# Performance work log

Measured on AMD Instinct MI355X. Metric: run time of the kernel, lower is better.

## Reference

```python
import jax, jax.numpy as jnp
import numpy as np

B, S, D = 8, 2048, 1024
H = 16
DH = D // H  # 64
DFF = 4 * D
EPS = 1e-5


def setup_inputs() -> dict:
    key = jax.random.key(0)
    ks = jax.random.split(key, 12)
    s = 0.02
    x = jax.random.normal(ks[0], (B, S, D), dtype=jnp.float32)
    mask = jnp.ones((B, S), dtype=bool)
    Wq = jax.random.normal(ks[1], (H, D, DH), dtype=jnp.float32) * s
    Wk = jax.random.normal(ks[2], (H, D, DH), dtype=jnp.float32) * s
    Wv = jax.random.normal(ks[3], (H, D, DH), dtype=jnp.float32) * s
    bq = jnp.zeros((H, DH), dtype=jnp.float32)
    bk = jnp.zeros((H, DH), dtype=jnp.float32)
    bv = jnp.zeros((H, DH), dtype=jnp.float32)
    Wo = jax.random.normal(ks[4], (D, D), dtype=jnp.float32) * s
    bo = jnp.zeros((D,), dtype=jnp.float32)
    W1 = jax.random.normal(ks[5], (D, DFF), dtype=jnp.float32) * s
    b1 = jnp.zeros((DFF,), dtype=jnp.float32)
    W2 = jax.random.normal(ks[6], (DFF, D), dtype=jnp.float32) * s
    b2 = jnp.zeros((D,), dtype=jnp.float32)
    ln1_w = jnp.ones((D,), dtype=jnp.float32)
    ln1_b = jnp.zeros((D,), dtype=jnp.float32)
    ln2_w = jnp.ones((D,), dtype=jnp.float32)
    ln2_b = jnp.zeros((D,), dtype=jnp.float32)
    return dict(x=x, mask=mask, Wq=Wq, bq=bq, Wk=Wk, bk=bk, Wv=Wv, bv=bv,
                Wo=Wo, bo=bo, W1=W1, b1=b1, W2=W2, b2=b2,
                ln1_w=ln1_w, ln1_b=ln1_b, ln2_w=ln2_w, ln2_b=ln2_b)


def _layernorm(x, w, b):
    m = jnp.mean(x, axis=-1, keepdims=True)
    v = jnp.mean(jnp.square(x - m), axis=-1, keepdims=True)
    return (x - m) * jax.lax.rsqrt(v + EPS) * w + b


def _mha(h, mask, Wq, bq, Wk, bk, Wv, bv, Wo, bo):
    # batched per-head projections: [B,S,D] x [H,D,DH] -> [B,H,S,DH]
    q = jnp.einsum('bsd,hde->bhse', h, Wq) + bq[None, :, None, :]
    k = jnp.einsum('bsd,hde->bhse', h, Wk) + bk[None, :, None, :]
    v = jnp.einsum('bsd,hde->bhse', h, Wv) + bv[None, :, None, :]
    scores = jnp.einsum('bhse,bhte->bhst', q, k) / np.sqrt(DH).astype(np.float32)
    scores = jnp.where(mask[:, None, None, :], scores, -1e9)
    w = jax.nn.softmax(scores, axis=-1)
    o = jnp.einsum('bhst,bhte->bhse', w, v)           # [B,H,S,DH]
    o = o.transpose(0, 2, 1, 3).reshape(o.shape[0], o.shape[2], -1)  # concat heads -> [B,S,D]
    return o @ Wo + bo


def reference(x, mask, Wq, bq, Wk, bk, Wv, bv, Wo, bo, W1, b1, W2, b2,
              ln1_w, ln1_b, ln2_w, ln2_b):
    h = _layernorm(x, ln1_w, ln1_b)
    x = x + _mha(h, mask, Wq, bq, Wk, bk, Wv, bv, Wo, bo)
    h2 = _layernorm(x, ln2_w, ln2_b)
    ff = jax.nn.gelu(h2 @ W1 + b1, approximate=False) @ W2 + b2  # dropout is identity in eval
    return x + ff
```

## Files before the change

### kernel.cpp

```cpp
#include <hip/hip_runtime.h>
#include <hip/hip_bf16.h>

#define DEV __device__ __forceinline__

typedef __attribute__((ext_vector_type(8))) short short8;
typedef __attribute__((ext_vector_type(4))) float floatx4;
typedef __attribute__((ext_vector_type(4))) short short4_t;
typedef __attribute__((ext_vector_type(4))) int int4_t;
typedef __attribute__((ext_vector_type(4))) float f4_t;

constexpr int S_ = 2048;
constexpr int D_ = 1024;
constexpr int M_ = 8 * 2048;
constexpr long QKV_ONE = 16384L * 1024L;

constexpr float QSCALE = 0.18033688011112042f;
constexpr float EXP2_BIAS = 5.770780163555851f;

DEV short f2bf(float f) {
  __hip_bfloat16 h = __float2bfloat16(f);
  return __builtin_bit_cast(short, h);
}

DEV int cvt_pk_bf16(float lo, float hi) {
  int r;
  asm("v_cvt_pk_bf16_f32 %0, %1, %2" : "=v"(r) : "v"(lo), "v"(hi));
  return r;
}

DEV void async16(const void* g, void* l) {
  __builtin_amdgcn_global_load_lds((const __attribute__((address_space(1))) void*)g,
                                   (__attribute__((address_space(3))) void*)l, 16, 0, 0);
}

DEV float gelu_exact(float x) {
  return 0.5f * x * (1.f + erff(x * 0.70710678118654752f));
}

#define SB0 __builtin_amdgcn_sched_barrier(0)
#define BARX { SB0; __builtin_amdgcn_s_barrier(); SB0; }
#define LGKM0 { asm volatile("s_waitcnt lgkmcnt(0)" ::: "memory"); SB0; }
#define WAITV(N) { asm volatile("s_waitcnt vmcnt(" #N ")" ::: "memory"); SB0; }


__global__ void pack_qkv_w(const float* __restrict__ Wq, const float* __restrict__ Wk,
                           const float* __restrict__ Wv, short* __restrict__ dst) {
  int idx = blockIdx.x * 256 + threadIdx.x;
  if (idx >= 3072 * 1024) return;
  int n = idx >> 10, k = idx & 1023;
  int which = n >> 10, hh = (n >> 6) & 15, e = n & 63;
  const float* W = (which == 0) ? Wq : ((which == 1) ? Wk : Wv);
  dst[idx] = f2bf(W[(hh * 1024 + k) * 64 + e]);
}

__global__ void pack_transpose(const float* __restrict__ src, short* __restrict__ dst,
                               int R, int C) {
  int idx = blockIdx.x * 256 + threadIdx.x;
  if (idx >= R * C) return;
  int r = idx % R, c = idx / R;
  dst[idx] = f2bf(src[(size_t)r * C + c]);
}

__global__ void pack_bias(const float* __restrict__ bq, const float* __restrict__ bk,
                          const float* __restrict__ bv, float* __restrict__ dst) {
  int idx = blockIdx.x * 256 + threadIdx.x;
  if (idx >= 3072) return;
  int which = idx >> 10;
  const float* b = (which == 0) ? bq : ((which == 1) ? bk : bv);
  dst[idx] = b[idx & 1023];
}


__global__ __launch_bounds__(256) void ln_kernel(const float* __restrict__ x,
                                                 const float* __restrict__ w,
                                                 const float* __restrict__ b,
                                                 short* __restrict__ out) {
  const int row = blockIdx.x * 4 + (threadIdx.x >> 6);
  const int lane = threadIdx.x & 63;
  const float* xr = x + (size_t)row * D_;
  f4_t v[4];
  float s1 = 0.f, s2 = 0.f;
#pragma unroll
  for (int k = 0; k < 4; ++k) {
    v[k] = *(const f4_t*)(xr + lane * 4 + k * 256);
    s1 += v[k].x + v[k].y + v[k].z + v[k].w;
    s2 += v[k].x * v[k].x + v[k].y * v[k].y + v[k].z * v[k].z + v[k].w * v[k].w;
  }
#pragma unroll
  for (int off = 32; off >= 1; off >>= 1) {
    s1 += __shfl_xor(s1, off);
    s2 += __shfl_xor(s2, off);
  }
  const float mean = s1 * (1.f / 1024.f);
  const float var = s2 * (1.f / 1024.f) - mean * mean;
  const float rstd = rsqrtf(var + 1e-5f);
#pragma unroll
  for (int k = 0; k < 4; ++k) {
    f4_t wv4 = *(const f4_t*)(w + lane * 4 + k * 256);
    f4_t bv4 = *(const f4_t*)(b + lane * 4 + k * 256);
    short4_t o;
    o[0] = f2bf((v[k].x - mean) * rstd * wv4.x + bv4.x);
    o[1] = f2bf((v[k].y - mean) * rstd * wv4.y + bv4.y);
    o[2] = f2bf((v[k].z - mean) * rstd * wv4.z + bv4.z);
    o[3] = f2bf((v[k].w - mean) * rstd * wv4.w + bv4.w);
    *(short4_t*)(out + (size_t)row * D_ + lane * 4 + k * 256) = o;
  }
}

template <int EPI>
__global__ __launch_bounds__(512, 2) void gemm256(const short* __restrict__ A,
                                                  const short* __restrict__ Bt,
                                                  const float* __restrict__ bias,
                                                  const float* __restrict__ res,
                                                  float* __restrict__ outf,
                                                  short* __restrict__ outb,
                                                  int M, int N, int K) {
  __shared__ short lds[32768];
  const int tid = threadIdx.x, lane = tid & 63, wv = tid >> 6;
  const int ln = lane & 15, quad = lane >> 4;
  const int wm = wv >> 2, wn = wv & 3;

  const int nbx = N >> 8;
  const int cpx = (int)gridDim.x >> 3;
  const int swz = ((int)blockIdx.x & 7) * cpx + ((int)blockIdx.x >> 3);
  const int bx = swz % nbx, by = swz / nbx;
  const int m0 = by << 8, n0 = bx << 8;

  const int grow = tid >> 2;
  const int gch8 = ((tid & 3) ^ ((tid >> 2) & 3)) << 3;
  const short* pA = A + (size_t)(m0 + grow) * K + gch8;
  const short* pB = Bt + (size_t)(n0 + grow) * K + gch8;
  char* const L = (char*)lds;
  const int ldst = wv << 10;

  const int cof = (quad ^ (ln & 3)) << 4;
  const int rA = (wm * 128 + ln) << 6;
  const int rB = (wn * 64 + ln) << 6;

  floatx4 acc[8][4];
#pragma unroll
  for (int i = 0; i < 8; ++i)
#pragma unroll
    for (int j = 0; j < 4; ++j) acc[i][j] = floatx4{0.f, 0.f, 0.f, 0.f};

  const int NT = K >> 5;

#pragma unroll
  for (int g = 0; g < 2; ++g) async16(pA + (size_t)(g * 128) * K, L + g * 8192 + ldst);
#pragma unroll
  for (int g = 0; g < 2; ++g) async16(pB + (size_t)(g * 128) * K, L + 32768 + g * 8192 + ldst);
#pragma unroll
  for (int g = 0; g < 2; ++g) async16(pB + (size_t)(g * 128) * K + 32, L + 49152 + g * 8192 + ldst);
  WAITV(2);
  BARX;

  for (int t = 0; t < NT; ++t) {
    const char* Ac = L + ((t & 1) << 14);
    const char* Bc = L + 32768 + ((t & 1) << 14);
    char* An = L + (((t + 1) & 1) << 14);
    char* Bn = L + 32768 + ((t & 1) << 14);
    const int kA = (t + 1) << 5;
    const int kB = (t + 2) << 5;

    if (t + 1 < NT) {
      async16(pA + kA, An + ldst);
      async16(pA + (size_t)128 * K + kA, An + 8192 + ldst);
    }
    short8 af[8], bf[4];
#pragma unroll
    for (int m = 0; m < 8; ++m) af[m] = *(const short8*)(Ac + rA + m * 1024 + cof);
#pragma unroll
    for (int n = 0; n < 4; ++n) bf[n] = *(const short8*)(Bc + rB + n * 1024 + cof);
    __builtin_amdgcn_s_setprio(1);
#pragma unroll
    for (int m = 0; m < 8; ++m)
      acc[m][0] = __builtin_amdgcn_mfma_f32_16x16x32_bf16(af[m], bf[0], acc[m][0], 0, 0, 0);
#pragma unroll
    for (int m = 0; m < 8; ++m)
      acc[m][1] = __builtin_amdgcn_mfma_f32_16x16x32_bf16(af[m], bf[1], acc[m][1], 0, 0, 0);
    __builtin_amdgcn_s_setprio(0);
    LGKM0;
    BARX;
    if (t + 2 < NT) {
      async16(pB + kB, Bn + ldst);
      async16(pB + (size_t)128 * K + kB, Bn + 8192 + ldst);
      WAITV(2);
    } else if (t + 1 < NT) {
      WAITV(0);
    }
    BARX;
    __builtin_amdgcn_s_setprio(1);
#pragma unroll
    for (int m = 0; m < 8; ++m)
      acc[m][2] = __builtin_amdgcn_mfma_f32_16x16x32_bf16(af[m], bf[2], acc[m][2], 0, 0, 0);
#pragma unroll
    for (int m = 0; m < 8; ++m)
      acc[m][3] = __builtin_amdgcn_mfma_f32_16x16x32_bf16(af[m], bf[3], acc[m][3], 0, 0, 0);
    __builtin_amdgcn_s_setprio(0);
  }

#pragma unroll
  for (int i = 0; i < 8; ++i) {
#pragma unroll
    for (int j = 0; j < 4; ++j) {
      const int n = n0 + wn * 64 + j * 16 + ln;
      const float bn = bias[n];
#pragma unroll
      for (int r = 0; r < 4; ++r) {
        const int m = m0 + wm * 128 + i * 16 + quad * 4 + r;
        float val = acc[i][j][r] + bn;
        if (EPI == 0) {
          int which = n >> 10, rem = n & 1023;
          int hh = rem >> 6, e = rem & 63;
          int bb = m >> 11, s = m & 2047;
          float v2 = (which == 0) ? val * QSCALE : val;
          outb[(size_t)which * QKV_ONE + (((size_t)(bb * 16 + hh) * 2048 + s) * 64 + e)] =
              f2bf(v2);
        } else if (EPI == 1) {
          outb[(size_t)m * N + n] = f2bf(gelu_exact(val));
        } else {
          outf[(size_t)m * N + n] = val + res[(size_t)m * N + n];
        }
      }
    }
  }
}

__global__ __launch_bounds__(256) void flash_attn(const short* __restrict__ Q,
                                                  const short* __restrict__ K,
                                                  const short* __restrict__ V,
                                                  short* __restrict__ O) {
  const int flat = blockIdx.x;
  const int xcd = flat & 7, slot = flat >> 3;
  const int bh = xcd * 16 + (slot >> 4);
  const int qb = slot & 15;
  const int b = bh >> 4, h = bh & 15;
  const int tid = threadIdx.x, lane = tid & 63, wv = tid >> 6;
  const int ln = lane & 15, quad = lane >> 4;

  __shared__ short Ks[64 * 64];
  __shared__ short Vt[64 * 64];

  const size_t base = (size_t)bh * S_ * 64;
  const int q0 = qb * 128 + wv * 32;

  const int s_ = ln >> 2, r_ = ln & 3;
  int tpm[2];
#pragma unroll
  for (int tp = 0; tp < 2; ++tp) {
    int d = tp * 2 + (r_ >> 1);
    tpm[tp] = 8 * ((s_ - d) & 3) + 2 * d + (r_ & 1);
  }
  int srcl[4];
#pragma unroll
  for (int d = 1; d < 4; ++d) srcl[d] = ((quad + d) & 3) * 16 + ln;

  short8 aq[2][2];
#pragma unroll
  for (int qt = 0; qt < 2; ++qt) {
    const short* qp = Q + base + (size_t)(q0 + qt * 16 + ln) * 64;
    aq[qt][0] = *(const short8*)(qp + quad * 8);
    aq[qt][1] = *(const short8*)(qp + 32 + quad * 8);
  }

  short8 ones;
#pragma unroll
  for (int ii = 0; ii < 8; ++ii) ones[ii] = (short)0x3F80;

  floatx4 oacc[2][4];
  floatx4 l_acc[2];
#pragma unroll
  for (int qt = 0; qt < 2; ++qt) {
    l_acc[qt] = floatx4{0.f, 0.f, 0.f, 0.f};
#pragma unroll
    for (int e4 = 0; e4 < 4; ++e4) oacc[qt][e4] = floatx4{0.f, 0.f, 0.f, 0.f};
  }

  for (int kb = 0; kb < S_; kb += 64) {
    __syncthreads();
#pragma unroll
    for (int i = 0; i < 2; ++i) {
      int sbase = wv * 64 + i * 256;
      int s = sbase + lane;
      int t = s >> 3;
      int gc = (s & 7) ^ ((t ^ (t >> 2)) & 7);
      async16(K + base + (size_t)(kb + t) * 64 + gc * 8, (char*)Ks + sbase * 16);
    }
    {
      int t = lane, e0 = wv * 16;
      const short* vp = V + base + (size_t)(kb + t) * 64 + e0;
      short8 v0 = *(const short8*)vp;
      short8 v1 = *(const short8*)(vp + 8);
      int c = t >> 3, o = t & 7;
#pragma unroll
      for (int ii = 0; ii < 8; ++ii) {
        int e = e0 + ii;
        Vt[e * 64 + ((c ^ (e & 7)) * 8) + o] = v0[ii];
      }
#pragma unroll
      for (int ii = 0; ii < 8; ++ii) {
        int e = e0 + 8 + ii;
        Vt[e * 64 + ((c ^ (e & 7)) * 8) + o] = v1[ii];
      }
    }
    __syncthreads();

#pragma unroll
    for (int g = 0; g < 2; ++g) {
      int pk[2][2][2];
#pragma unroll
      for (int tp = 0; tp < 2; ++tp) {
        int row = g * 32 + tpm[tp];
        int hsh = (row ^ (row >> 2)) & 7;
        short8 ak0 = *(const short8*)&Ks[row * 64 + ((quad ^ hsh) * 8)];
        short8 ak1 = *(const short8*)&Ks[row * 64 + (((4 + quad) ^ hsh) * 8)];
#pragma unroll
        for (int qt = 0; qt < 2; ++qt) {
          floatx4 s4 = floatx4{-EXP2_BIAS, -EXP2_BIAS, -EXP2_BIAS, -EXP2_BIAS};
          s4 = __builtin_amdgcn_mfma_f32_16x16x32_bf16(ak0, aq[qt][0], s4, 0, 0, 0);
          s4 = __builtin_amdgcn_mfma_f32_16x16x32_bf16(ak1, aq[qt][1], s4, 0, 0, 0);
          float p0 = __builtin_amdgcn_exp2f(s4[0]);
          float p1 = __builtin_amdgcn_exp2f(s4[1]);
          float p2 = __builtin_amdgcn_exp2f(s4[2]);
          float p3 = __builtin_amdgcn_exp2f(s4[3]);
          pk[qt][tp][0] = cvt_pk_bf16(p0, p1);
          pk[qt][tp][1] = cvt_pk_bf16(p2, p3);
        }
      }
      short8 bpq[2];
#pragma unroll
      for (int qt = 0; qt < 2; ++qt) {
        int4_t bw;
        bw[0] = pk[qt][0][0];
        bw[1] = __shfl(pk[qt][0][1], srcl[1], 64);
        bw[2] = __shfl(pk[qt][1][0], srcl[2], 64);
        bw[3] = __shfl(pk[qt][1][1], srcl[3], 64);
        bpq[qt] = __builtin_bit_cast(short8, bw);
        l_acc[qt] = __builtin_amdgcn_mfma_f32_16x16x32_bf16(ones, bpq[qt], l_acc[qt], 0, 0, 0);
      }
#pragma unroll
      for (int e4 = 0; e4 < 4; ++e4) {
        int e = e4 * 16 + ln;
        short8 av = *(const short8*)&Vt[e * 64 + (((g * 4 + quad) ^ (e & 7)) * 8)];
        oacc[0][e4] = __builtin_amdgcn_mfma_f32_16x16x32_bf16(av, bpq[0], oacc[0][e4], 0, 0, 0);
        oacc[1][e4] = __builtin_amdgcn_mfma_f32_16x16x32_bf16(av, bpq[1], oacc[1][e4], 0, 0, 0);
      }
    }
  }

#pragma unroll
  for (int qt = 0; qt < 2; ++qt) {
    float linv = __builtin_amdgcn_rcpf(l_acc[qt][0]);
    size_t rowbase = ((size_t)b * S_ + q0 + qt * 16 + ln) * D_ + h * 64;
#pragma unroll
    for (int e4 = 0; e4 < 4; ++e4) {
      short4_t o;
#pragma unroll
      for (int r = 0; r < 4; ++r) o[r] = f2bf(oacc[qt][e4][r] * linv);
      *(short4_t*)&O[rowbase + e4 * 16 + quad * 4] = o;
    }
  }
}


extern "C" void kernel_launch(void* const* d_in, const int* in_sizes, int n_in,
                              void* d_out, int out_size, void* d_ws, size_t ws_size,
                              hipStream_t stream) {
  const float* x    = (const float*)d_in[0];
  const float* Wq   = (const float*)d_in[2];
  const float* bq   = (const float*)d_in[3];
  const float* Wk   = (const float*)d_in[4];
  const float* bk   = (const float*)d_in[5];
  const float* Wv   = (const float*)d_in[6];
  const float* bv   = (const float*)d_in[7];
  const float* Wo   = (const float*)d_in[8];
  const float* bo   = (const float*)d_in[9];
  const float* W1   = (const float*)d_in[10];
  const float* b1   = (const float*)d_in[11];
  const float* W2   = (const float*)d_in[12];
  const float* b2   = (const float*)d_in[13];
  const float* ln1w = (const float*)d_in[14];
  const float* ln1b = (const float*)d_in[15];
  const float* ln2w = (const float*)d_in[16];
  const float* ln2b = (const float*)d_in[17];
  float* out = (float*)d_out;

  char* ws = (char*)d_ws;
  short* Wqkv_t = (short*)(ws + 0);
  short* Wo_t   = (short*)(ws + 6291456);
  short* W1_t   = (short*)(ws + 8388608);
  short* W2_t   = (short*)(ws + 16777216);
  float* bqkv   = (float*)(ws + 25165824);
  short* hbuf   = (short*)(ws + 25178112);
  short* qkv    = (short*)(ws + 58732544);
  short* obuf   = (short*)(ws + 159395840);
  short* ff1    = qkv;

  pack_qkv_w<<<(3072 * 1024 + 255) / 256, 256, 0, stream>>>(Wq, Wk, Wv, Wqkv_t);
  pack_transpose<<<(1024 * 1024 + 255) / 256, 256, 0, stream>>>(Wo, Wo_t, 1024, 1024);
  pack_transpose<<<(1024 * 4096 + 255) / 256, 256, 0, stream>>>(W1, W1_t, 1024, 4096);
  pack_transpose<<<(4096 * 1024 + 255) / 256, 256, 0, stream>>>(W2, W2_t, 4096, 1024);
  pack_bias<<<12, 256, 0, stream>>>(bq, bk, bv, bqkv);

  ln_kernel<<<M_ / 4, 256, 0, stream>>>(x, ln1w, ln1b, hbuf);

  gemm256<0><<<dim3(768), 512, 0, stream>>>(
      hbuf, Wqkv_t, bqkv, nullptr, nullptr, qkv, M_, 3072, 1024);

  flash_attn<<<dim3(2048), 256, 0, stream>>>(
      qkv, qkv + QKV_ONE, qkv + 2 * QKV_ONE, obuf);

  gemm256<2><<<dim3(256), 512, 0, stream>>>(
      obuf, Wo_t, bo, x, out, nullptr, M_, 1024, 1024);

  ln_kernel<<<M_ / 4, 256, 0, stream>>>(out, ln2w, ln2b, hbuf);

  gemm256<1><<<dim3(1024), 512, 0, stream>>>(
      hbuf, W1_t, b1, nullptr, nullptr, ff1, M_, 4096, 1024);

  gemm256<2><<<dim3(256), 512, 0, stream>>>(
      ff1, W2_t, b2, out, out, nullptr, M_, 1024, 4096);
}
```

Before: 931.3 us.

## Triple-buffer GEMM LDS tiles with two-stage-ahead prefetch and new swizzle

Expands the GEMM shared-memory buffer to hold three stages each of A and B tiles, and issues global-to-LDS loads two K-steps ahead for both operands using rotating buffer offsets. It removes the explicit lgkmcnt wait before the mid-loop barrier and changes the XOR swizzle of the LDS chunk layout to use bits 2-3 of the row. The aim is to hide more global-load latency and reduce LDS bank conflicts. In exchange, LDS use grows to 96 KB per block, which may cut occupancy below the two blocks per CU requested by the launch bounds.

```diff
diff --git a/kernel.cpp b/kernel.cpp
--- a/kernel.cpp
+++ b/kernel.cpp
@@ -39,7 +39,6 @@
 
 #define SB0 __builtin_amdgcn_sched_barrier(0)
 #define BARX { SB0; __builtin_amdgcn_s_barrier(); SB0; }
-#define LGKM0 { asm volatile("s_waitcnt lgkmcnt(0)" ::: "memory"); SB0; }
 #define WAITV(N) { asm volatile("s_waitcnt vmcnt(" #N ")" ::: "memory"); SB0; }
 
 
@@ -115,7 +114,7 @@
                                                   float* __restrict__ outf,
                                                   short* __restrict__ outb,
                                                   int M, int N, int K) {
-  __shared__ short lds[32768];
+  __shared__ short lds[49152];
   const int tid = threadIdx.x, lane = tid & 63, wv = tid >> 6;
   const int ln = lane & 15, quad = lane >> 4;
   const int wm = wv >> 2, wn = wv & 3;
@@ -127,13 +126,13 @@
   const int m0 = by << 8, n0 = bx << 8;
 
   const int grow = tid >> 2;
-  const int gch8 = ((tid & 3) ^ ((tid >> 2) & 3)) << 3;
+  const int gch8 = ((tid & 3) ^ ((tid >> 4) & 3)) << 3;
   const short* pA = A + (size_t)(m0 + grow) * K + gch8;
   const short* pB = Bt + (size_t)(n0 + grow) * K + gch8;
   char* const L = (char*)lds;
   const int ldst = wv << 10;
 
-  const int cof = (quad ^ (ln & 3)) << 4;
+  const int cof = (quad ^ ((ln >> 2) & 3)) << 4;
   const int rA = (wm * 128 + ln) << 6;
   const int rB = (wn * 64 + ln) << 6;
 
@@ -148,29 +147,28 @@
 #pragma unroll
   for (int g = 0; g < 2; ++g) async16(pA + (size_t)(g * 128) * K, L + g * 8192 + ldst);
 #pragma unroll
-  for (int g = 0; g < 2; ++g) async16(pB + (size_t)(g * 128) * K, L + 32768 + g * 8192 + ldst);
-#pragma unroll
-  for (int g = 0; g < 2; ++g) async16(pB + (size_t)(g * 128) * K + 32, L + 49152 + g * 8192 + ldst);
-  WAITV(2);
+  for (int g = 0; g < 2; ++g) async16(pB + (size_t)(g * 128) * K, L + 49152 + g * 8192 + ldst);
+#pragma unroll
+  for (int g = 0; g < 2; ++g) async16(pA + (size_t)(g * 128) * K + 32, L + 16384 + g * 8192 + ldst);
+#pragma unroll
+  for (int g = 0; g < 2; ++g) async16(pB + (size_t)(g * 128) * K + 32, L + 65536 + g * 8192 + ldst);
+  WAITV(4);
   BARX;
 
+  int aC = 0, aN = 16384, aN2 = 32768;
+  int bC = 49152, bN = 65536, bN2 = 81920;
+
   for (int t = 0; t < NT; ++t) {
-    const char* Ac = L + ((t & 1) << 14);
-    const char* Bc = L + 32768 + ((t & 1) << 14);
-    char* An = L + (((t + 1) & 1) << 14);
-    char* Bn = L + 32768 + ((t & 1) << 14);
-    const int kA = (t + 1) << 5;
-    const int kB = (t + 2) << 5;
-
-    if (t + 1 < NT) {
-      async16(pA + kA, An + ldst);
-      async16(pA + (size_t)128 * K + kA, An + 8192 + ldst);
+    const int kS = (t + 2) << 5;
+    if (t + 2 < NT) {
+      async16(pA + kS, L + aN2 + ldst);
+      async16(pA + (size_t)128 * K + kS, L + aN2 + 8192 + ldst);
     }
     short8 af[8], bf[4];
 #pragma unroll
-    for (int m = 0; m < 8; ++m) af[m] = *(const short8*)(Ac + rA + m * 1024 + cof);
-#pragma unroll
-    for (int n = 0; n < 4; ++n) bf[n] = *(const short8*)(Bc + rB + n * 1024 + cof);
+    for (int m = 0; m < 8; ++m) af[m] = *(const short8*)(L + aC + rA + m * 1024 + cof);
+#pragma unroll
+    for (int n = 0; n < 4; ++n) bf[n] = *(const short8*)(L + bC + rB + n * 1024 + cof);
     __builtin_amdgcn_s_setprio(1);
 #pragma unroll
     for (int m = 0; m < 8; ++m)
@@ -179,13 +177,12 @@
     for (int m = 0; m < 8; ++m)
       acc[m][1] = __builtin_amdgcn_mfma_f32_16x16x32_bf16(af[m], bf[1], acc[m][1], 0, 0, 0);
     __builtin_amdgcn_s_setprio(0);
-    LGKM0;
     BARX;
     if (t + 2 < NT) {
-      async16(pB + kB, Bn + ldst);
-      async16(pB + (size_t)128 * K + kB, Bn + 8192 + ldst);
-      WAITV(2);
-    } else if (t + 1 < NT) {
+      async16(pB + kS, L + bN2 + ldst);
+      async16(pB + (size_t)128 * K + kS, L + bN2 + 8192 + ldst);
+      WAITV(4);
+    } else {
       WAITV(0);
     }
     BARX;
@@ -197,6 +194,8 @@
     for (int m = 0; m < 8; ++m)
       acc[m][3] = __builtin_amdgcn_mfma_f32_16x16x32_bf16(af[m], bf[3], acc[m][3], 0, 0, 0);
     __builtin_amdgcn_s_setprio(0);
+    int tmp = aC; aC = aN; aN = aN2; aN2 = tmp;
+    tmp = bC; bC = bN; bN = bN2; bN2 = tmp;
   }
 
 #pragma unroll
```

Measured after the change: 934.5 us. Within noise of the previous version (+0.3%).
